# Kernel tuning notes

Hardware: AMD Instinct MI355X
Metric: run time of the kernel (lower is better)

## Reference

```python
import jax, jax.numpy as jnp
import numpy as np

B = 131072
D_IN = 128
D_H = 128


def _linear_params(key, fan_in, fan_out):
    # mimic nn.Linear init: U(-1/sqrt(fan_in), 1/sqrt(fan_in))
    kw, kb = jax.random.split(key)
    bound = 1.0 / np.sqrt(fan_in)
    W = jax.random.uniform(kw, (fan_in, fan_out), minval=-bound, maxval=bound, dtype=jnp.float32)
    b = jax.random.uniform(kb, (fan_out,), minval=-bound, maxval=bound, dtype=jnp.float32)
    return W, b


def setup_inputs() -> dict:
    key = jax.random.key(0)
    ks = jax.random.split(key, 12)
    inp = {
        'input': jax.random.normal(ks[0], (B, D_IN), dtype=jnp.float32),
        'seq_input': jax.random.normal(ks[1], (B, D_IN), dtype=jnp.float32),
        'hidden': jax.random.normal(ks[2], (B, D_H), dtype=jnp.float32),
    }
    names = ['ir', 'iz', 'in_', 'sr', 'sz', 'sn', 'hr', 'hz', 'hn']
    for i, nm in enumerate(names):
        fan_in = D_H if nm.startswith('h') else D_IN
        W, b = _linear_params(ks[3 + i], fan_in, D_H)
        inp['W_' + nm] = W
        inp['b_' + nm] = b
    return inp


def reference(input, seq_input, hidden,
              W_ir, b_ir, W_iz, b_iz, W_in_, b_in_,
              W_sr, b_sr, W_sz, b_sz, W_sn, b_sn,
              W_hr, b_hr, W_hz, b_hz, W_hn, b_hn):
    def lin(x, W, b):
        return x @ W + b

    hr = lin(hidden, W_hr, b_hr)  # shared between r_input and r_seq
    r_input = jax.nn.sigmoid(lin(input, W_ir, b_ir) + hr)
    r_seq = jax.nn.sigmoid(lin(seq_input, W_sr, b_sr) + hr)
    r = (r_input + r_seq) * 0.5

    hz = lin(hidden, W_hz, b_hz)
    z_input = jax.nn.sigmoid(lin(input, W_iz, b_iz) + hz)
    z_seq = jax.nn.sigmoid(lin(seq_input, W_sz, b_sz) + hz)
    z = (z_input + z_seq) * 0.5

    n = jnp.tanh(lin(input, W_in_, b_in_) + lin(seq_input, W_sn, b_sn)
                 + lin(r * hidden, W_hn, b_hn))
    new_hidden = (1.0 - z) * n + z * hidden
    return new_hidden
```

## Files before the change

kernel.cpp:

```cpp
#include <hip/hip_runtime.h>

#define BDIM 512
#define PACK_BDIM 256

typedef __attribute__((ext_vector_type(8))) short bf16x8;
typedef __attribute__((ext_vector_type(4))) float f32x4;
typedef __attribute__((ext_vector_type(4))) unsigned int u32x4;

__device__ __forceinline__ unsigned short f2b(float x) {
    unsigned u = __float_as_uint(x);
    return (unsigned short)((u + 0x7fffu + ((u >> 16) & 1u)) >> 16);
}
__device__ __forceinline__ float b2f(unsigned short b) {
    return __uint_as_float(((unsigned)b) << 16);
}

typedef __attribute__((address_space(1))) const unsigned int ga_u32;
typedef __attribute__((address_space(3))) unsigned int la_u32;
__device__ __forceinline__ void gload_lds16(const void* g, void* l) {
    __builtin_amdgcn_global_load_lds((ga_u32*)g, (la_u32*)l, 16, 0, 0);
}

__global__ __launch_bounds__(PACK_BDIM) void pack_weights(
    const float* __restrict__ w0, const float* __restrict__ w1,
    const float* __restrict__ w2, const float* __restrict__ w3,
    const float* __restrict__ w4, const float* __restrict__ w5,
    const float* __restrict__ w6, const float* __restrict__ w7,
    const float* __restrict__ w8, unsigned short* __restrict__ wp)
{
    __shared__ float wsm[16384];
    const float* W;
    switch (blockIdx.x) {
        case 0: W = w0; break; case 1: W = w1; break; case 2: W = w2; break;
        case 3: W = w3; break; case 4: W = w4; break; case 5: W = w5; break;
        case 6: W = w6; break; case 7: W = w7; break; default: W = w8; break;
    }
    const int tid = threadIdx.x;
    for (int i = tid; i < 16384; i += PACK_BDIM) wsm[i] = W[i];
    __syncthreads();
    unsigned short* dst = wp + (size_t)blockIdx.x * 32768;
    for (int item = tid; item < 4096; item += PACK_BDIM) {
        const int lane = item & 63, q = item >> 6;
        const int s = q >> 5, cf = q & 31, c = cf >> 3, f = cf & 7;
        const int k0 = c * 32 + (lane >> 4) * 8;
        const int n  = f * 16 + (lane & 15);
        unsigned v2[4];
        for (int i2 = 0; i2 < 4; i2++) {
            unsigned short lohi[2];
            for (int t = 0; t < 2; t++) {
                float x = wsm[(k0 + i2 * 2 + t) * 128 + n];
                unsigned short hb = f2b(x);
                if (s) { hb = (unsigned short)(__float_as_uint(x - b2f(hb)) >> 16); }
                lohi[t] = hb;
            }
            v2[i2] = (unsigned)lohi[0] | ((unsigned)lohi[1] << 16);
        }
        u32x4 vv; vv[0] = v2[0]; vv[1] = v2[1]; vv[2] = v2[2]; vv[3] = v2[3];
        *(u32x4*)(dst + (size_t)(s * 32 + cf) * 512 + lane * 8) = vv;
    }
}

__global__ __launch_bounds__(BDIM, 2) void gru_fused(
    const float* __restrict__ inp, const float* __restrict__ seqp,
    const float* __restrict__ hid, const unsigned short* __restrict__ wp,
    const float* __restrict__ b_ir, const float* __restrict__ b_iz,
    const float* __restrict__ b_in, const float* __restrict__ b_sr,
    const float* __restrict__ b_sz, const float* __restrict__ b_sn,
    const float* __restrict__ b_hr, const float* __restrict__ b_hz,
    const float* __restrict__ b_hn, float* __restrict__ outp)
{
    __shared__ __align__(16) unsigned short whbuf[16384];
    float* tb = (float*)whbuf;

    const int tid    = threadIdx.x;
    const int lane   = tid & 63;
    const int wid    = tid >> 6;
    const int rowgrp = wid >> 1;
    const int colgrp = wid & 1;
    const int agrp   = lane >> 4;
    const int a16    = lane & 15;
    const int ncol0  = colgrp * 64;
    const size_t row0 = (size_t)blockIdx.x * 64;
    const int locrow_a = rowgrp * 16 + a16;
    const int rswA = (locrow_a & 7) << 3;

    const float* pAin  = inp  + (row0 + locrow_a) * 128;
    const float* pAseq = seqp + (row0 + locrow_a) * 128;
    const float* pAhid = hid  + (row0 + locrow_a) * 128;

    f32x4 hx[4], t[4], s1[4], nacc[4], rA[8];
    const f32x4 zv = {0.f, 0.f, 0.f, 0.f};

    auto stage = [&](int g, int s) {
        const char* src = (const char*)wp + (size_t)g * 65536 + (size_t)s * 32768;
        #pragma unroll
        for (int j = 0; j < 4; j++) {
            const int off = (j * 8 + wid) * 1024;
            gload_lds16(src + off + lane * 16, (char*)whbuf + off);
        }
    };

    auto phase = [&](int g, f32x4* acc, const float* pA, const f32x4* rAv, bool init) {
        __syncthreads();
        stage(g, 0);
        bf16x8 ah[4], al[4];
        #pragma unroll
        for (int c = 0; c < 4; c++) {
            const float* p = pA + c * 32 + agrp * 8;
            f32x4 x0 = *(const f32x4*)(p);
            f32x4 x1 = *(const f32x4*)(p + 4);
            if (rAv) { x0 *= rAv[2 * c]; x1 *= rAv[2 * c + 1]; }
            #pragma unroll
            for (int i = 0; i < 4; i++) {
                unsigned short hb = f2b(x0[i]);
                ah[c][i] = (short)hb;
                al[c][i] = (short)(__float_as_uint(x0[i] - b2f(hb)) >> 16);
                unsigned short hb1 = f2b(x1[i]);
                ah[c][4 + i] = (short)hb1;
                al[c][4 + i] = (short)(__float_as_uint(x1[i] - b2f(hb1)) >> 16);
            }
        }
        if (init) {
            #pragma unroll
            for (int f = 0; f < 4; f++) acc[f] = zv;
        }
        __syncthreads();
        #pragma unroll
        for (int c = 0; c < 4; c++)
            #pragma unroll
            for (int f = 0; f < 4; f++) {
                const int fglob = colgrp * 4 + f;
                const bf16x8 wh = *(const bf16x8*)(&whbuf[(size_t)(c * 8 + fglob) * 512 + lane * 8]);
                acc[f] = __builtin_amdgcn_mfma_f32_16x16x32_bf16(ah[c], wh, acc[f], 0, 0, 0);
                acc[f] = __builtin_amdgcn_mfma_f32_16x16x32_bf16(al[c], wh, acc[f], 0, 0, 0);
            }
        __syncthreads();
        stage(g, 1);
        __syncthreads();
        #pragma unroll
        for (int c = 0; c < 4; c++)
            #pragma unroll
            for (int f = 0; f < 4; f++) {
                const int fglob = colgrp * 4 + f;
                const bf16x8 wl = *(const bf16x8*)(&whbuf[(size_t)(c * 8 + fglob) * 512 + lane * 8]);
                acc[f] = __builtin_amdgcn_mfma_f32_16x16x32_bf16(ah[c], wl, acc[f], 0, 0, 0);
            }
    };

    auto addb = [&](f32x4* acc, const float* b) {
        #pragma unroll
        for (int f = 0; f < 4; f++) {
            float bv = b[ncol0 + f * 16 + a16];
            #pragma unroll
            for (int j = 0; j < 4; j++) acc[f][j] += bv;
        }
    };

    auto sigm = [](float x) { return 1.f / (1.f + __expf(-x)); };
    auto tanh_ = [](float x) {
        x = fminf(18.f, fmaxf(-18.f, x));
        float e = __expf(2.f * x);
        return (e - 1.f) / (e + 1.f);
    };

    phase(6, hx, pAhid, nullptr, true); addb(hx, b_hr);
    phase(0, t, pAin, nullptr, true);  addb(t, b_ir);
    #pragma unroll
    for (int f = 0; f < 4; f++)
        #pragma unroll
        for (int j = 0; j < 4; j++) s1[f][j] = sigm(t[f][j] + hx[f][j]);
    phase(3, t, pAseq, nullptr, true); addb(t, b_sr);

    __syncthreads();
    #pragma unroll
    for (int f = 0; f < 4; f++)
        #pragma unroll
        for (int j = 0; j < 4; j++) {
            int row = rowgrp * 16 + agrp * 4 + j;
            int col = ncol0 + f * 16 + a16;
            tb[row * 128 + (col ^ ((row & 7) << 3))] =
                0.5f * (s1[f][j] + sigm(t[f][j] + hx[f][j]));
        }
    __syncthreads();
    #pragma unroll
    for (int c = 0; c < 4; c++) {
        int rk = (c * 32 + agrp * 8) ^ rswA;
        rA[2 * c]     = *(const f32x4*)(&tb[locrow_a * 128 + rk]);
        rA[2 * c + 1] = *(const f32x4*)(&tb[locrow_a * 128 + rk + 4]);
    }

    phase(8, nacc, pAhid, rA, true);      addb(nacc, b_hn);
    phase(2, nacc, pAin, nullptr, false);  addb(nacc, b_in);
    phase(5, nacc, pAseq, nullptr, false); addb(nacc, b_sn);

    phase(7, hx, pAhid, nullptr, true); addb(hx, b_hz);
    phase(1, t, pAin, nullptr, true);  addb(t, b_iz);
    #pragma unroll
    for (int f = 0; f < 4; f++)
        #pragma unroll
        for (int j = 0; j < 4; j++) s1[f][j] = sigm(t[f][j] + hx[f][j]);
    phase(4, t, pAseq, nullptr, true); addb(t, b_sz);

    __syncthreads();
    #pragma unroll
    for (int f = 0; f < 4; f++)
        #pragma unroll
        for (int j = 0; j < 4; j++) {
            int row = rowgrp * 16 + agrp * 4 + j;
            int col = ncol0 + f * 16 + a16;
            float zz = 0.5f * (s1[f][j] + sigm(t[f][j] + hx[f][j]));
            float h  = hid[(row0 + row) * 128 + col];
            float nn = tanh_(nacc[f][j]);
            tb[row * 128 + (col ^ ((row & 7) << 3))] = (1.f - zz) * nn + zz * h;
        }
    __syncthreads();
    #pragma unroll
    for (int p = 0; p < 4; p++) {
        int e = p * 2048 + tid * 4;
        int rrow = e >> 7, c0 = e & 127;
        f32x4 v = *(const f32x4*)(&tb[rrow * 128 + (c0 ^ ((rrow & 7) << 3))]);
        *(f32x4*)(&outp[(row0 + rrow) * 128 + c0]) = v;
    }
}

extern "C" void kernel_launch(void* const* d_in, const int* in_sizes, int n_in,
                              void* d_out, int out_size, void* d_ws, size_t ws_size,
                              hipStream_t stream)
{
    (void)in_sizes; (void)n_in; (void)out_size; (void)ws_size;
    const float* inp  = (const float*)d_in[0];
    const float* seqp = (const float*)d_in[1];
    const float* hid  = (const float*)d_in[2];
    const float* W[9]; const float* Bv[9];
    for (int i = 0; i < 9; i++) {
        W[i]  = (const float*)d_in[3 + 2 * i];
        Bv[i] = (const float*)d_in[4 + 2 * i];
    }
    unsigned short* wp = (unsigned short*)d_ws;

    pack_weights<<<9, PACK_BDIM, 0, stream>>>(W[0], W[1], W[2], W[3], W[4],
                                              W[5], W[6], W[7], W[8], wp);
    gru_fused<<<2048, BDIM, 0, stream>>>(inp, seqp, hid, wp,
                                         Bv[0], Bv[1], Bv[2], Bv[3], Bv[4],
                                         Bv[5], Bv[6], Bv[7], Bv[8],
                                         (float*)d_out);
}
```

Before: 312.1 us.

## Double-buffer weight staging in LDS and use truncation for bf16 hi/lo split

Splits each GEMM phase into a hi-weight pass and a lo-weight pass over two LDS buffers. Each pass prefetches the next weight slab into the other buffer while it computes, which removes the load-then-wait stalls and cuts the number of barriers per phase. The bf16 high part of each activation is now produced by bit truncation instead of round-to-nearest, which saves ALU work; the residual term still carries the lost bits. In exchange, LDS use per block doubles to 64KB, and launch bounds become waves_per_eu(4), which may change occupancy or register allocation.

```diff
diff --git a/kernel.cpp b/kernel.cpp
--- a/kernel.cpp
+++ b/kernel.cpp
@@ -60,7 +60,8 @@
     }
 }
 
-__global__ __launch_bounds__(BDIM, 2) void gru_fused(
+__global__ __launch_bounds__(BDIM) __attribute__((amdgpu_waves_per_eu(4)))
+void gru_fused(
     const float* __restrict__ inp, const float* __restrict__ seqp,
     const float* __restrict__ hid, const unsigned short* __restrict__ wp,
     const float* __restrict__ b_ir, const float* __restrict__ b_iz,
@@ -69,8 +70,8 @@
     const float* __restrict__ b_hr, const float* __restrict__ b_hz,
     const float* __restrict__ b_hn, float* __restrict__ outp)
 {
-    __shared__ __align__(16) unsigned short whbuf[16384];
-    float* tb = (float*)whbuf;
+    __shared__ __align__(16) unsigned short wbuf[2][16384];
+    float* tb = (float*)wbuf[1];
 
     const int tid    = threadIdx.x;
     const int lane   = tid & 63;
@@ -89,21 +90,21 @@
     const float* pAhid = hid  + (row0 + locrow_a) * 128;
 
     f32x4 hx[4], t[4], s1[4], nacc[4], rA[8];
+    bf16x8 ahs[4];
     const f32x4 zv = {0.f, 0.f, 0.f, 0.f};
 
-    auto stage = [&](int g, int s) {
+    auto stageu = [&](int g, int s, int b) {
         const char* src = (const char*)wp + (size_t)g * 65536 + (size_t)s * 32768;
+        char* dstb = (char*)wbuf[b];
         #pragma unroll
         for (int j = 0; j < 4; j++) {
             const int off = (j * 8 + wid) * 1024;
-            gload_lds16(src + off + lane * 16, (char*)whbuf + off);
-        }
-    };
-
-    auto phase = [&](int g, f32x4* acc, const float* pA, const f32x4* rAv, bool init) {
-        __syncthreads();
-        stage(g, 0);
-        bf16x8 ah[4], al[4];
+            gload_lds16(src + off + lane * 16, dstb + off);
+        }
+    };
+
+    auto hiU = [&](f32x4* acc, const float* pA, const f32x4* rAv, bool init) {
+        bf16x8 al[4];
         #pragma unroll
         for (int c = 0; c < 4; c++) {
             const float* p = pA + c * 32 + agrp * 8;
@@ -112,38 +113,41 @@
             if (rAv) { x0 *= rAv[2 * c]; x1 *= rAv[2 * c + 1]; }
             #pragma unroll
             for (int i = 0; i < 4; i++) {
-                unsigned short hb = f2b(x0[i]);
-                ah[c][i] = (short)hb;
-                al[c][i] = (short)(__float_as_uint(x0[i] - b2f(hb)) >> 16);
-                unsigned short hb1 = f2b(x1[i]);
-                ah[c][4 + i] = (short)hb1;
-                al[c][4 + i] = (short)(__float_as_uint(x1[i] - b2f(hb1)) >> 16);
+                unsigned u0 = __float_as_uint(x0[i]);
+                ahs[c][i] = (short)(u0 >> 16);
+                float h0 = __uint_as_float(u0 & 0xffff0000u);
+                al[c][i] = (short)(__float_as_uint(x0[i] - h0) >> 16);
+                unsigned u1 = __float_as_uint(x1[i]);
+                ahs[c][4 + i] = (short)(u1 >> 16);
+                float h1 = __uint_as_float(u1 & 0xffff0000u);
+                al[c][4 + i] = (short)(__float_as_uint(x1[i] - h1) >> 16);
             }
         }
         if (init) {
             #pragma unroll
             for (int f = 0; f < 4; f++) acc[f] = zv;
         }
-        __syncthreads();
+        const unsigned short* wb = wbuf[0];
         #pragma unroll
         for (int c = 0; c < 4; c++)
             #pragma unroll
             for (int f = 0; f < 4; f++) {
                 const int fglob = colgrp * 4 + f;
-                const bf16x8 wh = *(const bf16x8*)(&whbuf[(size_t)(c * 8 + fglob) * 512 + lane * 8]);
-                acc[f] = __builtin_amdgcn_mfma_f32_16x16x32_bf16(ah[c], wh, acc[f], 0, 0, 0);
+                const bf16x8 wh = *(const bf16x8*)(&wb[(size_t)(c * 8 + fglob) * 512 + lane * 8]);
+                acc[f] = __builtin_amdgcn_mfma_f32_16x16x32_bf16(ahs[c], wh, acc[f], 0, 0, 0);
                 acc[f] = __builtin_amdgcn_mfma_f32_16x16x32_bf16(al[c], wh, acc[f], 0, 0, 0);
             }
-        __syncthreads();
-        stage(g, 1);
-        __syncthreads();
+    };
+
+    auto loU = [&](f32x4* acc) {
+        const unsigned short* wb = wbuf[1];
         #pragma unroll
         for (int c = 0; c < 4; c++)
             #pragma unroll
             for (int f = 0; f < 4; f++) {
                 const int fglob = colgrp * 4 + f;
-                const bf16x8 wl = *(const bf16x8*)(&whbuf[(size_t)(c * 8 + fglob) * 512 + lane * 8]);
-                acc[f] = __builtin_amdgcn_mfma_f32_16x16x32_bf16(ah[c], wl, acc[f], 0, 0, 0);
+                const bf16x8 wl = *(const bf16x8*)(&wb[(size_t)(c * 8 + fglob) * 512 + lane * 8]);
+                acc[f] = __builtin_amdgcn_mfma_f32_16x16x32_bf16(ahs[c], wl, acc[f], 0, 0, 0);
             }
     };
 
@@ -163,13 +167,24 @@
         return (e - 1.f) / (e + 1.f);
     };
 
-    phase(6, hx, pAhid, nullptr, true); addb(hx, b_hr);
-    phase(0, t, pAin, nullptr, true);  addb(t, b_ir);
+    stageu(6, 0, 0);
+
+    __syncthreads(); stageu(6, 1, 1);
+    hiU(hx, pAhid, nullptr, true);
+    __syncthreads(); stageu(0, 0, 0);
+    loU(hx); addb(hx, b_hr);
+    __syncthreads(); stageu(0, 1, 1);
+    hiU(t, pAin, nullptr, true);
+    __syncthreads(); stageu(3, 0, 0);
+    loU(t); addb(t, b_ir);
     #pragma unroll
     for (int f = 0; f < 4; f++)
         #pragma unroll
         for (int j = 0; j < 4; j++) s1[f][j] = sigm(t[f][j] + hx[f][j]);
-    phase(3, t, pAseq, nullptr, true); addb(t, b_sr);
+    __syncthreads(); stageu(3, 1, 1);
+    hiU(t, pAseq, nullptr, true);
+    __syncthreads(); stageu(8, 0, 0);
+    loU(t); addb(t, b_sr);
 
     __syncthreads();
     #pragma unroll
@@ -189,17 +204,34 @@
         rA[2 * c + 1] = *(const f32x4*)(&tb[locrow_a * 128 + rk + 4]);
     }
 
-    phase(8, nacc, pAhid, rA, true);      addb(nacc, b_hn);
-    phase(2, nacc, pAin, nullptr, false);  addb(nacc, b_in);
-    phase(5, nacc, pAseq, nullptr, false); addb(nacc, b_sn);
-
-    phase(7, hx, pAhid, nullptr, true); addb(hx, b_hz);
-    phase(1, t, pAin, nullptr, true);  addb(t, b_iz);
+    __syncthreads(); stageu(8, 1, 1);
+    hiU(nacc, pAhid, rA, true);
+    __syncthreads(); stageu(2, 0, 0);
+    loU(nacc); addb(nacc, b_hn);
+    __syncthreads(); stageu(2, 1, 1);
+    hiU(nacc, pAin, nullptr, false);
+    __syncthreads(); stageu(5, 0, 0);
+    loU(nacc); addb(nacc, b_in);
+    __syncthreads(); stageu(5, 1, 1);
+    hiU(nacc, pAseq, nullptr, false);
+    __syncthreads(); stageu(7, 0, 0);
+    loU(nacc); addb(nacc, b_sn);
+    __syncthreads(); stageu(7, 1, 1);
+    hiU(hx, pAhid, nullptr, true);
+    __syncthreads(); stageu(1, 0, 0);
+    loU(hx); addb(hx, b_hz);
+    __syncthreads(); stageu(1, 1, 1);
+    hiU(t, pAin, nullptr, true);
+    __syncthreads(); stageu(4, 0, 0);
+    loU(t); addb(t, b_iz);
     #pragma unroll
     for (int f = 0; f < 4; f++)
         #pragma unroll
         for (int j = 0; j < 4; j++) s1[f][j] = sigm(t[f][j] + hx[f][j]);
-    phase(4, t, pAseq, nullptr, true); addb(t, b_sz);
+    __syncthreads(); stageu(4, 1, 1);
+    hiU(t, pAseq, nullptr, true);
+    __syncthreads();
+    loU(t); addb(t, b_sz);
 
     __syncthreads();
     #pragma unroll
```

Measured after the change: 291.8 us. 6.5% less time.
